# Performance work log

Hardware: AMD Instinct MI355X
Metric: run time of the kernel (lower is better)

The kernel has to match this reference:

```python
import jax, jax.numpy as jnp
import numpy as np

B, S, D_MODEL = 8, 1024, 512
DIM_K = DIM_V = 512
N_HEADS = 8
DK = DIM_K // N_HEADS
DV = DIM_V // N_HEADS
NORM = 1.0 / np.sqrt(D_MODEL).astype(np.float32)  # note: 1/sqrt(d_model), per source


def setup_inputs() -> dict:
    key = jax.random.key(0)
    ks = jax.random.split(key, 6)
    s = 0.05  # small init to keep softmax well-conditioned
    return {
        "x": jax.random.normal(ks[0], (B, S, D_MODEL), jnp.float32),
        "y": jax.random.normal(ks[1], (B, S, D_MODEL), jnp.float32),
        "q_w": jax.random.normal(ks[2], (D_MODEL, DIM_K), jnp.float32) * s,
        "q_b": jnp.zeros((DIM_K,), jnp.float32),
        "k_w": jax.random.normal(ks[3], (D_MODEL, DIM_K), jnp.float32) * s,
        "k_b": jnp.zeros((DIM_K,), jnp.float32),
        "v_w": jax.random.normal(ks[4], (D_MODEL, DIM_V), jnp.float32) * s,
        "v_b": jnp.zeros((DIM_V,), jnp.float32),
        "o_w": jax.random.normal(ks[5], (DIM_V, D_MODEL), jnp.float32) * s,
        "o_b": jnp.zeros((D_MODEL,), jnp.float32),
    }


def reference(x, y, q_w, q_b, k_w, k_b, v_w, v_b, o_w, o_b):
    b, s, _ = x.shape
    # Faithful to torch: plain row-major reshape (B,S,dim) -> (H,B,S,dh),
    # NOT a per-token head split.
    Q = (x @ q_w + q_b).reshape(N_HEADS, b, s, DK)
    K = (y @ k_w + k_b).reshape(N_HEADS, b, s, DK)
    V = (y @ v_w + v_b).reshape(N_HEADS, b, s, DV)
    scores = jnp.einsum("hbqd,hbkd->hbqk", Q, K) * NORM  # [H,B,S,S]
    # dynamic mean-threshold mask: keep only scores strictly above row mean
    thre = jnp.mean(scores, axis=-1, keepdims=True)
    scores = jnp.where(scores > thre, scores, -jnp.inf)
    attn = jax.nn.softmax(scores, axis=-1)
    out = jnp.einsum("hbqk,hbkd->hbqd", attn, V).reshape(b, s, DIM_V)
    return out @ o_w + o_b
```

## Files before the change

kernel.cpp:

```cpp
#include <hip/hip_runtime.h>
#include <hip/hip_bf16.h>
#include <hip/hip_fp16.h>


typedef _Float16 f16;
typedef __attribute__((ext_vector_type(4))) _Float16 f16x4;
typedef __attribute__((ext_vector_type(8))) _Float16 f16x8;
typedef __attribute__((ext_vector_type(8))) short bf16x8;
typedef __attribute__((ext_vector_type(4))) float f32x4;

#define MFMA16(a, b, c) __builtin_amdgcn_mfma_f32_16x16x32_f16((a), (b), (c), 0, 0, 0)
#define MFMAB16(a, b, c) __builtin_amdgcn_mfma_f32_16x16x32_bf16((a), (b), (c), 0, 0, 0)
#define MFMAPV(a, b, c) __builtin_amdgcn_mfma_f32_16x16x16f16((a), (b), (c), 0, 0, 0)

#if defined(__has_builtin) && __has_builtin(__builtin_amdgcn_exp2f)
#define EXPFN(x) __builtin_amdgcn_exp2f(x)
#define QPROJ_SCALE (0.04419417382415922f * 1.4426950408889634f)
#else
#define EXPFN(x) __expf(x)
#define QPROJ_SCALE 0.04419417382415922f
#endif

#define GLL16(gp, lp)                                       \
  __builtin_amdgcn_global_load_lds(                         \
      (const __attribute__((address_space(1))) void*)(gp),  \
      (__attribute__((address_space(3))) void*)(lp), 16, 0, 0)

__device__ __forceinline__ float b2f(short s) {
  return __uint_as_float(((unsigned)(unsigned short)s) << 16);
}

__device__ __forceinline__ void splitbf(float v, short& h, short& l) {
  unsigned short hu = __bfloat16_as_ushort(__float2bfloat16(v));
  h = (short)hu;
  float hf = __uint_as_float(((unsigned)hu) << 16);
  l = (short)__bfloat16_as_ushort(__float2bfloat16(v - hf));
}

__global__ void k_wt(const float* __restrict__ w0, const float* __restrict__ w1,
                     const float* __restrict__ w2, const float* __restrict__ w3,
                     short* __restrict__ qh, short* __restrict__ ql,
                     short* __restrict__ kh, short* __restrict__ kl,
                     f16* __restrict__ vt, f16* __restrict__ ot) {
  const float* W;
  switch (blockIdx.z) {
    case 0: W = w0; break;
    case 1: W = w1; break;
    case 2: W = w2; break;
    default: W = w3; break;
  }
  __shared__ float t[32][33];
  int bx = blockIdx.x, by = blockIdx.y;
  int tx = threadIdx.x, ty = threadIdx.y;
#pragma unroll
  for (int i = 0; i < 32; i += 8)
    t[ty + i][tx] = W[(size_t)(by * 32 + ty + i) * 512 + bx * 32 + tx];
  __syncthreads();
#pragma unroll
  for (int i = 0; i < 32; i += 8) {
    size_t idx = (size_t)(bx * 32 + ty + i) * 512 + by * 32 + tx;
    float v = t[tx][ty + i];
    if (blockIdx.z < 2) {
      short h, l;
      splitbf(v, h, l);
      if (blockIdx.z == 0) { qh[idx] = h; ql[idx] = l; }
      else { kh[idx] = h; kl[idx] = l; }
    } else {
      if (blockIdx.z == 2) vt[idx] = (f16)v;
      else ot[idx] = (f16)v;
    }
  }
}

__global__ __launch_bounds__(256) void k_split(
    const float* __restrict__ x, const float* __restrict__ y,
    short* __restrict__ Xh, short* __restrict__ Xl, short* __restrict__ Yh,
    short* __restrict__ Yl, f16* __restrict__ Ym) {
  const float* src = blockIdx.y ? y : x;
  short* dh = blockIdx.y ? Yh : Xh;
  short* dl = blockIdx.y ? Yl : Xl;
  const size_t i = ((size_t)blockIdx.x * 256 + threadIdx.x) * 8;
  float4 a = *(const float4*)(src + i);
  float4 b = *(const float4*)(src + i + 4);
  float v[8] = {a.x, a.y, a.z, a.w, b.x, b.y, b.z, b.w};
  bf16x8 h, l;
#pragma unroll
  for (int j = 0; j < 8; ++j) {
    short hh, ll;
    splitbf(v[j], hh, ll);
    h[j] = hh;
    l[j] = ll;
  }
  *(bf16x8*)(dh + i) = h;
  *(bf16x8*)(dl + i) = l;
  if (blockIdx.y) {
    f16x8 m8;
#pragma unroll
    for (int j = 0; j < 8; ++j) m8[j] = (f16)v[j];
    *(f16x8*)(Ym + i) = m8;
  }
}

#define GSTAGE(buf, kk)                                              \
  {                                                                  \
    _Pragma("unroll") for (int j = 0; j < 4; ++j) {                  \
      const int rowu = half + j * 16;                                \
      const int row = rowu + srow;                                   \
      const int slog = sslot ^ ((row >> 1) & 3);                     \
      GLL16(gsb + (size_t)(rb + row) * 512 + (kk) + slog * 8,        \
            &ldsb[buf][rowu][0]);                                    \
    }                                                                \
  }

template <typename OT>
__device__ __forceinline__ void gemm16_gll(const f16* __restrict__ A,
                                           const f16* __restrict__ WT,
                                           const float* __restrict__ bias,
                                           OT* __restrict__ C, int m0, int n0,
                                           f16 (*As)[128][32],
                                           f16 (*Bs)[128][32]) {
  const int tid = threadIdx.x;
  const int wv = tid >> 6, lane = tid & 63;
  const int wm = wv >> 1, wn = wv & 1;
  const int l15 = lane & 15, lg = lane >> 4;
  const int srow = lane >> 2, sslot = lane & 3;

  const f16* gsb = (wv < 2) ? A : WT;
  const int rb = (wv < 2) ? m0 : n0;
  f16(*ldsb)[128][32] = (wv < 2) ? As : Bs;
  const int half = (wv & 1) * 64;

  const f32x4 fz = {0.f, 0.f, 0.f, 0.f};
  f32x4 acc[4][4];
#pragma unroll
  for (int m = 0; m < 4; ++m)
#pragma unroll
    for (int n = 0; n < 4; ++n) acc[m][n] = fz;

  GSTAGE(0, 0);
  int cur = 0;
  for (int k0 = 0; k0 < 512; k0 += 32) {
    __syncthreads();
    if (k0 < 480) GSTAGE(cur ^ 1, k0 + 32);
    f16x8 af[4], bf[4];
#pragma unroll
    for (int m = 0; m < 4; ++m) {
      const int r = wm * 64 + m * 16 + l15;
      af[m] = *(const f16x8*)&As[cur][r][(lg ^ ((r >> 1) & 3)) * 8];
    }
#pragma unroll
    for (int n = 0; n < 4; ++n) {
      const int r = wn * 64 + n * 16 + l15;
      bf[n] = *(const f16x8*)&Bs[cur][r][(lg ^ ((r >> 1) & 3)) * 8];
    }
#pragma unroll
    for (int m = 0; m < 4; ++m)
#pragma unroll
      for (int n = 0; n < 4; ++n) acc[m][n] = MFMA16(af[m], bf[n], acc[m][n]);
    cur ^= 1;
  }
#pragma unroll
  for (int n = 0; n < 4; ++n) {
    const int col = n0 + wn * 64 + n * 16 + l15;
    const float b = bias[col];
#pragma unroll
    for (int m = 0; m < 4; ++m) {
      const int row = m0 + wm * 64 + m * 16 + lg * 4;
#pragma unroll
      for (int r = 0; r < 4; ++r)
        C[(size_t)(row + r) * 512 + col] = (OT)(acc[m][n][r] + b);
    }
  }
}

__global__ __launch_bounds__(256) void k_gemm_out(const f16* __restrict__ Om,
                                                  const f16* __restrict__ owT,
                                                  const float* __restrict__ ob,
                                                  float* __restrict__ out) {
  __shared__ __align__(16) f16 As[2][128][32];
  __shared__ __align__(16) f16 Bs[2][128][32];
  const int lid = blockIdx.x + (blockIdx.y << 2);
  const int swz = ((lid & 7) << 5) + (lid >> 3);
  gemm16_gll<float>(Om, owT, ob, out, (swz >> 2) * 128, (swz & 3) * 128, As,
                    Bs);
}

#define PSTAGE(buf, kk)                                             \
  {                                                                 \
    _Pragma("unroll") for (int j = 0; j < 8; ++j) {                 \
      const int row = j * 16 + srow;                                \
      const int slog = sslot ^ ((row >> 1) & 3);                    \
      GLL16(gsb + (size_t)(rb + row) * 512 + (kk) + slog * 8,       \
            &sm4[buf][wv][j * 16][0]);                              \
    }                                                               \
  }

__global__ __launch_bounds__(256) void k_proj(
    const short* __restrict__ Xh, const short* __restrict__ Xl,
    const short* __restrict__ Yh, const short* __restrict__ Yl,
    const f16* __restrict__ Ym, const short* __restrict__ qwh,
    const short* __restrict__ qwl, const short* __restrict__ kwh,
    const short* __restrict__ kwl, const f16* __restrict__ vwT,
    const float* __restrict__ qb, const float* __restrict__ kbias,
    const float* __restrict__ vb, short* __restrict__ Qh,
    short* __restrict__ Ql, short* __restrict__ Kh, short* __restrict__ Kl,
    f16* __restrict__ Vm, float* __restrict__ Kpart) {
  __shared__ __align__(16) short sm4[2][4][128][32];
  const int lid = blockIdx.x + (blockIdx.y << 2);
  const int swz = ((lid & 7) << 5) + (lid >> 3);
  const int nt = swz & 3, mt = swz >> 2;
  const int m0 = mt * 128, n0 = nt * 128;
  const int z = blockIdx.z;
  if (z == 2) {
    gemm16_gll<f16>(Ym, vwT, vb, Vm, m0, n0, (f16(*)[128][32]) & sm4[0][0][0][0],
                    (f16(*)[128][32]) & sm4[0][2][0][0]);
    return;
  }
  const short* Agh = z ? Yh : Xh;
  const short* Agl = z ? Yl : Xl;
  const short* Wh = z ? kwh : qwh;
  const short* Wl = z ? kwl : qwl;
  const float* bias = z ? kbias : qb;
  short* Ch = z ? Kh : Qh;
  short* Cl = z ? Kl : Ql;
  const float osc = z ? 1.f : (float)QPROJ_SCALE;

  const int tid = threadIdx.x;
  const int wv = tid >> 6, lane = tid & 63;
  const int wm = wv >> 1, wn = wv & 1;
  const int l15 = lane & 15, lg = lane >> 4;
  const int srow = lane >> 2, sslot = lane & 3;

  const short* gsb = (wv == 0) ? Agh : (wv == 1) ? Agl : (wv == 2) ? Wh : Wl;
  const int rb = (wv < 2) ? m0 : n0;

  const f32x4 fz = {0.f, 0.f, 0.f, 0.f};
  f32x4 acc[4][4];
#pragma unroll
  for (int m = 0; m < 4; ++m)
#pragma unroll
    for (int n = 0; n < 4; ++n) acc[m][n] = fz;

  PSTAGE(0, 0);
  int cur = 0;
  for (int k0 = 0; k0 < 512; k0 += 32) {
    __syncthreads();
    if (k0 < 480) PSTAGE(cur ^ 1, k0 + 32);
    bf16x8 afh[4], afl[4], bfh[4], bfl[4];
#pragma unroll
    for (int m = 0; m < 4; ++m) {
      const int r = wm * 64 + m * 16 + l15;
      const int sl = (lg ^ ((r >> 1) & 3)) * 8;
      afh[m] = *(const bf16x8*)&sm4[cur][0][r][sl];
      afl[m] = *(const bf16x8*)&sm4[cur][1][r][sl];
    }
#pragma unroll
    for (int n = 0; n < 4; ++n) {
      const int r = wn * 64 + n * 16 + l15;
      const int sl = (lg ^ ((r >> 1) & 3)) * 8;
      bfh[n] = *(const bf16x8*)&sm4[cur][2][r][sl];
      bfl[n] = *(const bf16x8*)&sm4[cur][3][r][sl];
    }
#pragma unroll
    for (int m = 0; m < 4; ++m)
#pragma unroll
      for (int n = 0; n < 4; ++n) {
        acc[m][n] = MFMAB16(afh[m], bfh[n], acc[m][n]);
        acc[m][n] = MFMAB16(afh[m], bfl[n], acc[m][n]);
        acc[m][n] = MFMAB16(afl[m], bfh[n], acc[m][n]);
      }
    cur ^= 1;
  }
  float csum[4];
#pragma unroll
  for (int n = 0; n < 4; ++n) {
    const int col = n0 + wn * 64 + n * 16 + l15;
    const float b = bias[col];
    csum[n] = 16.f * b;
#pragma unroll
    for (int m = 0; m < 4; ++m) {
      const int row = m0 + wm * 64 + m * 16 + lg * 4;
#pragma unroll
      for (int r = 0; r < 4; ++r) {
        const float vraw = acc[m][n][r] + b;
        csum[n] += acc[m][n][r];
        short h, l;
        splitbf(vraw * osc, h, l);
        const size_t idx = (size_t)(row + r) * 512 + col;
        Ch[idx] = h;
        Cl[idx] = l;
      }
    }
  }
  if (z == 1) {
    float* cred = (float*)&sm4[0][0][0][0];
    __syncthreads();
#pragma unroll
    for (int n = 0; n < 4; ++n)
      cred[(wn * 64 + n * 16 + l15) * 8 + wm * 4 + lg] = csum[n];
    __syncthreads();
    if (tid < 64) {
      float s = 0.f;
#pragma unroll
      for (int j = 0; j < 8; ++j)
        s += cred[tid * 8 + j] + cred[(tid + 64) * 8 + j];
      Kpart[((size_t)mt * 4 + nt) * 64 + tid] = s;
    }
  }
}

__global__ __launch_bounds__(256) void k_vtr(const f16* __restrict__ Vm,
                                             f16* __restrict__ Vt) {
  const int p = blockIdx.y;
  const int j0 = blockIdx.x * 16;
  __shared__ f16 L[16][520];
  const int tid = threadIdx.x;
#pragma unroll
  for (int it = 0; it < 4; ++it) {
    int idx = it * 256 + tid;
    int row = idx >> 6, oct = idx & 63;
    *(f16x8*)&L[row][oct * 8] =
        *(const f16x8*)&Vm[(size_t)(p * 128 + j0 + row) * 512 + oct * 8];
  }
  __syncthreads();
#pragma unroll
  for (int it = 0; it < 4; ++it) {
    int idx = it * 256 + tid;
    int dh = idx >> 4, j = idx & 15;
    f16x8 v;
#pragma unroll
    for (int g = 0; g < 8; ++g) v[g] = L[j][g * 64 + dh];
    *(f16x8*)&Vt[((size_t)p * 64 + dh) * 1024 + (j0 + j) * 8] = v;
  }
}

#define LOADREG(cc)                              \
  {                                              \
    rh = *(const bf16x8*)(KhSrc + (cc) * 4096);  \
    rl = *(const bf16x8*)(KlSrc + (cc) * 4096);  \
    rv = *(const f16x8*)(VSrc + (cc) * 64);      \
  }
#define STOREBUF(b)                      \
  {                                      \
    *(bf16x8*)&KhS[b][skey][sslot] = rh; \
    *(bf16x8*)&KlS[b][skey][sslot] = rl; \
    *(f16x8*)&Vs[b][skey][sslot] = rv;   \
  }

#define CHUNK(cb_, c_)                                                        \
  {                                                                           \
    __syncthreads();                                                          \
    if ((c_) < 15) STOREBUF((cb_) ^ 1);             \
    if ((c_) < 14) LOADREG((c_) + 2);                                         \
    __builtin_amdgcn_s_setprio(1);                                            \
    f32x4 aa[4];                                                              \
    _Pragma("unroll") for (int t = 0; t < 4; ++t) {                           \
      const int krow = t * 16 + l15;                                          \
      const int ksw = l15 & 7;                           \
      bf16x8 kh0 = *(const bf16x8*)&KhS[cb_][krow][(lg ^ ksw) * 8];           \
      bf16x8 kh1 = *(const bf16x8*)&KhS[cb_][krow][((4 + lg) ^ ksw) * 8];     \
      bf16x8 kl0 = *(const bf16x8*)&KlS[cb_][krow][(lg ^ ksw) * 8];           \
      bf16x8 kl1 = *(const bf16x8*)&KlS[cb_][krow][((4 + lg) ^ ksw) * 8];     \
      f32x4 s1 = fz, s2 = fz;                                                 \
      s1 = MFMAB16(kh0, qh0, s1);                                             \
      s2 = MFMAB16(kh1, qh1, s2);                                             \
      s1 = MFMAB16(kl0, qh0, s1);                                             \
      s2 = MFMAB16(kl1, qh1, s2);                                             \
      s1 = MFMAB16(kh0, ql0, s1);                                             \
      s2 = MFMAB16(kh1, ql1, s2);                                             \
      aa[t] = s1 + s2;                                                        \
    }                                                                         \
    f16x4 va[4][4];                                                           \
    _Pragma("unroll") for (int d0 = 0; d0 < 4; ++d0) {                        \
      const int vrow = d0 * 16 + l15;                                         \
      const int vsw = l15 & 7;                                                \
      _Pragma("unroll") for (int t = 0; t < 4; ++t)                           \
        va[d0][t] = *(const f16x4*)&Vs[cb_][vrow]                             \
                        [(((t * 2 + (lg >> 1)) ^ vsw) * 8) + (lg & 1) * 4];   \
    }                                                                         \
    f16x4 pf[4];                                                              \
    _Pragma("unroll") for (int t = 0; t < 4; ++t)                             \
      _Pragma("unroll") for (int r = 0; r < 4; ++r) {                         \
        float v = aa[t][r];                                                   \
        pf[t][r] = (f16)((v > sm) ? EXPFN(v) : 0.f);                          \
      }                                                                       \
    _Pragma("unroll") for (int t = 0; t < 4; ++t) {                           \
      od = MFMAPV(kones, pf[t], od);                                          \
      _Pragma("unroll") for (int d0 = 0; d0 < 4; ++d0)                        \
        oac[d0] = MFMAPV(va[d0][t], pf[t], oac[d0]);                          \
    }                                                                         \
    __builtin_amdgcn_s_setprio(0);                                            \
  }

__global__ __launch_bounds__(512, 4) void k_attn(
    const short* __restrict__ Qh, const short* __restrict__ Ql,
    const short* __restrict__ Kh, const short* __restrict__ Kl,
    const f16* __restrict__ Vt, const float* __restrict__ Kpart,
    f16* __restrict__ Om) {
  constexpr int S = 1024, DH = 64;
  const int p = blockIdx.x;
  const int qt = blockIdx.y;
  const size_t pb = (size_t)p * S * DH;
  const short* Qhp = Qh + pb;
  const short* Qlp = Ql + pb;
  const short* Khp = Kh + pb;
  const short* Klp = Kl + pb;
  const f16* Vtp = Vt + pb;
  f16* Op = Om + pb;

  const int tid = threadIdx.x;
  const int w = tid >> 6, lane = tid & 63;
  const int l15 = lane & 15, lg = lane >> 4;

  __shared__ __align__(16) short KhS[2][64][64];
  __shared__ __align__(16) short KlS[2][64][64];
  __shared__ __align__(16) f16 Vs[2][64][64];

  const int skey = tid >> 3;
  const int slot8 = tid & 7;
  const int sslot = (slot8 ^ (skey & 7)) * 8;
  const short* KhSrc = Khp + skey * 64 + slot8 * 8;
  const short* KlSrc = Klp + skey * 64 + slot8 * 8;
  const f16* VSrc = Vtp + (size_t)skey * 1024 + slot8 * 8;

  bf16x8 rh, rl;
  f16x8 rv;
  LOADREG(0);
  STOREBUF(0);
  LOADREG(1);

  const int qrow = qt * 128 + w * 16;
  const size_t qo = (size_t)(qrow + l15) * DH + lg * 8;
  bf16x8 qh0 = *(const bf16x8*)(Qhp + qo);
  bf16x8 ql0 = *(const bf16x8*)(Qlp + qo);
  bf16x8 qh1 = *(const bf16x8*)(Qhp + qo + 32);
  bf16x8 ql1 = *(const bf16x8*)(Qlp + qo + 32);

  const float* kp = Kpart + (size_t)p * 256;
  float km0[8], km1[8];
#pragma unroll
  for (int j = 0; j < 8; ++j) { km0[j] = 0.f; km1[j] = 0.f; }
#pragma unroll
  for (int pt = 0; pt < 4; ++pt) {
    const float* bb = kp + pt * 64;
#pragma unroll
    for (int j = 0; j < 8; ++j) {
      km0[j] += bb[lg * 8 + j];
      km1[j] += bb[32 + lg * 8 + j];
    }
  }
  float sm = 0.f;
#pragma unroll
  for (int j = 0; j < 8; ++j) {
    sm += (b2f(qh0[j]) + b2f(ql0[j])) * km0[j] +
          (b2f(qh1[j]) + b2f(ql1[j])) * km1[j];
  }
  sm += __shfl_xor(sm, 16);
  sm += __shfl_xor(sm, 32);
  sm *= (1.f / 1024.f);

  const f32x4 fz = {0.f, 0.f, 0.f, 0.f};
  const f16x4 kones = {(f16)1.f, (f16)1.f, (f16)1.f, (f16)1.f};
  f32x4 oac[4];
#pragma unroll
  for (int d = 0; d < 4; ++d) oac[d] = fz;
  f32x4 od = fz;

  for (int cc = 0; cc < 16; cc += 2) {
    CHUNK(0, cc);
    CHUNK(1, cc + 1);
  }

  const float inv = 1.f / od[0];
#pragma unroll
  for (int d0 = 0; d0 < 4; ++d0) {
    f16x4 o0;
#pragma unroll
    for (int r = 0; r < 4; ++r) o0[r] = (f16)(oac[d0][r] * inv);
    *(f16x4*)&Op[(size_t)(qrow + l15) * DH + d0 * 16 + lg * 4] = o0;
  }
}

extern "C" void kernel_launch(void* const* d_in, const int* in_sizes, int n_in,
                              void* d_out, int out_size, void* d_ws,
                              size_t ws_size, hipStream_t stream) {
  const float* x = (const float*)d_in[0];
  const float* y = (const float*)d_in[1];
  const float* qw = (const float*)d_in[2];
  const float* qb = (const float*)d_in[3];
  const float* kw = (const float*)d_in[4];
  const float* kbias = (const float*)d_in[5];
  const float* vw = (const float*)d_in[6];
  const float* vb = (const float*)d_in[7];
  const float* ow = (const float*)d_in[8];
  const float* ob = (const float*)d_in[9];
  float* out = (float*)d_out;

  char* ws = (char*)d_ws;
  const size_t WT_B = 512ull * 512 * 2;
  const size_t MAT_B = 8192ull * 512 * 2;
  short* qwhT = (short*)(ws + 0 * WT_B);
  short* qwlT = (short*)(ws + 1 * WT_B);
  short* kwhT = (short*)(ws + 2 * WT_B);
  short* kwlT = (short*)(ws + 3 * WT_B);
  f16* vwT = (f16*)(ws + 4 * WT_B);
  f16* owT = (f16*)(ws + 5 * WT_B);
  char* m = ws + 6 * WT_B;
  short* Qh = (short*)(m + 0 * MAT_B);
  short* Ql = (short*)(m + 1 * MAT_B);
  short* Kh = (short*)(m + 2 * MAT_B);
  short* Kl = (short*)(m + 3 * MAT_B);
  f16* Vm = (f16*)(m + 4 * MAT_B);
  short* Xh = (short*)(m + 5 * MAT_B);
  short* Xl = (short*)(m + 6 * MAT_B);
  short* Yh = (short*)(m + 7 * MAT_B);
  short* Yl = (short*)(m + 8 * MAT_B);
  f16* Ym = (f16*)(m + 9 * MAT_B);
  float* Kpart = (float*)(m + 10 * MAT_B);
  f16* Vtr = (f16*)Xh;
  f16* Om = (f16*)Yh;

  hipLaunchKernelGGL(k_wt, dim3(16, 16, 4), dim3(32, 8), 0, stream, qw, kw, vw,
                     ow, qwhT, qwlT, kwhT, kwlT, vwT, owT);
  hipLaunchKernelGGL(k_split, dim3(2048, 2), dim3(256), 0, stream, x, y, Xh,
                     Xl, Yh, Yl, Ym);
  hipLaunchKernelGGL(k_proj, dim3(4, 64, 3), dim3(256), 0, stream, Xh, Xl, Yh,
                     Yl, Ym, qwhT, qwlT, kwhT, kwlT, vwT, qb, kbias, vb, Qh,
                     Ql, Kh, Kl, Vm, Kpart);
  hipLaunchKernelGGL(k_vtr, dim3(8, 64), dim3(256), 0, stream, Vm, Vtr);
  hipLaunchKernelGGL(k_attn, dim3(64, 8), dim3(512), 0, stream, Qh, Ql, Kh,
                     Kl, Vtr, Kpart, Om);
  hipLaunchKernelGGL(k_gemm_out, dim3(4, 64), dim3(256), 0, stream, Om, owT,
                     ob, out);
}
```

Baseline: 118.4 us.

## Fuse weight prep into split kernel, use async LDS loads in attention, retile output GEMM

Merges the weight transpose/convert kernel into the input split kernel so a single launch handles both. The attention kernel's K/V staging switches from register load-then-store to direct global-to-LDS loads, with the swizzle moved to the source address. The output GEMM moves from 128x128 to 128x64 tiles with a dedicated staging macro, doubling the block count to improve occupancy. The aims are fewer launches, lower register pressure, and better CU fill, at the cost of uneven work in the fused prep kernel.

```diff
diff --git a/kernel.cpp b/kernel.cpp
--- a/kernel.cpp
+++ b/kernel.cpp
@@ -37,49 +37,48 @@
   l = (short)__bfloat16_as_ushort(__float2bfloat16(v - hf));
 }
 
-__global__ void k_wt(const float* __restrict__ w0, const float* __restrict__ w1,
-                     const float* __restrict__ w2, const float* __restrict__ w3,
-                     short* __restrict__ qh, short* __restrict__ ql,
-                     short* __restrict__ kh, short* __restrict__ kl,
-                     f16* __restrict__ vt, f16* __restrict__ ot) {
-  const float* W;
-  switch (blockIdx.z) {
-    case 0: W = w0; break;
-    case 1: W = w1; break;
-    case 2: W = w2; break;
-    default: W = w3; break;
-  }
-  __shared__ float t[32][33];
-  int bx = blockIdx.x, by = blockIdx.y;
-  int tx = threadIdx.x, ty = threadIdx.y;
-#pragma unroll
-  for (int i = 0; i < 32; i += 8)
-    t[ty + i][tx] = W[(size_t)(by * 32 + ty + i) * 512 + bx * 32 + tx];
-  __syncthreads();
-#pragma unroll
-  for (int i = 0; i < 32; i += 8) {
-    size_t idx = (size_t)(bx * 32 + ty + i) * 512 + by * 32 + tx;
-    float v = t[tx][ty + i];
-    if (blockIdx.z < 2) {
-      short h, l;
-      splitbf(v, h, l);
-      if (blockIdx.z == 0) { qh[idx] = h; ql[idx] = l; }
-      else { kh[idx] = h; kl[idx] = l; }
-    } else {
-      if (blockIdx.z == 2) vt[idx] = (f16)v;
-      else ot[idx] = (f16)v;
-    }
-  }
-}
-
-__global__ __launch_bounds__(256) void k_split(
+__global__ __launch_bounds__(256) void k_pre(
     const float* __restrict__ x, const float* __restrict__ y,
+    const float* __restrict__ qw, const float* __restrict__ kw,
+    const float* __restrict__ vw, const float* __restrict__ ow,
+    short* __restrict__ qh, short* __restrict__ ql, short* __restrict__ kh,
+    short* __restrict__ kl, f16* __restrict__ vt, f16* __restrict__ ot,
     short* __restrict__ Xh, short* __restrict__ Xl, short* __restrict__ Yh,
     short* __restrict__ Yl, f16* __restrict__ Ym) {
-  const float* src = blockIdx.y ? y : x;
-  short* dh = blockIdx.y ? Yh : Xh;
-  short* dl = blockIdx.y ? Yl : Xl;
-  const size_t i = ((size_t)blockIdx.x * 256 + threadIdx.x) * 8;
+  const int tid = threadIdx.x;
+  const int bx = blockIdx.x;
+  const int by = blockIdx.y;
+  if (bx < 512) {
+    const int wt = by * 512 + bx;
+    const int z = wt >> 8;
+    const int tile = wt & 255;
+    const int bxx = tile & 15, byy = tile >> 4;
+    const float* W = (z == 0) ? qw : (z == 1) ? kw : (z == 2) ? vw : ow;
+    __shared__ float t[32][33];
+    const int tx = tid & 31, ty = tid >> 5;
+#pragma unroll
+    for (int i = 0; i < 32; i += 8)
+      t[ty + i][tx] = W[(size_t)(byy * 32 + ty + i) * 512 + bxx * 32 + tx];
+    __syncthreads();
+#pragma unroll
+    for (int i = 0; i < 32; i += 8) {
+      size_t idx = (size_t)(bxx * 32 + ty + i) * 512 + byy * 32 + tx;
+      float v = t[tx][ty + i];
+      if (z < 2) {
+        short h, l;
+        splitbf(v, h, l);
+        if (z == 0) { qh[idx] = h; ql[idx] = l; }
+        else { kh[idx] = h; kl[idx] = l; }
+      } else {
+        if (z == 2) vt[idx] = (f16)v;
+        else ot[idx] = (f16)v;
+      }
+    }
+  }
+  const float* src = by ? y : x;
+  short* dh = by ? Yh : Xh;
+  short* dl = by ? Yl : Xl;
+  const size_t i = ((size_t)bx * 256 + tid) * 8;
   float4 a = *(const float4*)(src + i);
   float4 b = *(const float4*)(src + i + 4);
   float v[8] = {a.x, a.y, a.z, a.w, b.x, b.y, b.z, b.w};
@@ -93,7 +92,7 @@
   }
   *(bf16x8*)(dh + i) = h;
   *(bf16x8*)(dl + i) = l;
-  if (blockIdx.y) {
+  if (by) {
     f16x8 m8;
 #pragma unroll
     for (int j = 0; j < 8; ++j) m8[j] = (f16)v[j];
@@ -173,16 +172,83 @@
   }
 }
 
+#define OSTAGE(buf, kk)                                                       \
+  {                                                                           \
+    if (wv < 2) {                                                             \
+      _Pragma("unroll") for (int j = 0; j < 4; ++j) {                         \
+        const int rowu = wv * 64 + j * 16;                                    \
+        const int row = rowu + srow;                                          \
+        const int slog = sslot ^ ((row >> 1) & 3);                            \
+        GLL16(Om + (size_t)(m0 + row) * 512 + (kk) + slog * 8,                \
+              &As[buf][rowu][0]);                                             \
+      }                                                                       \
+    } else {                                                                  \
+      _Pragma("unroll") for (int j = 0; j < 2; ++j) {                         \
+        const int rowu = (wv - 2) * 32 + j * 16;                              \
+        const int row = rowu + srow;                                          \
+        const int slog = sslot ^ ((row >> 1) & 3);                            \
+        GLL16(owT + (size_t)(n0 + row) * 512 + (kk) + slog * 8,               \
+              &Bs[buf][rowu][0]);                                             \
+      }                                                                       \
+    }                                                                         \
+  }
+
 __global__ __launch_bounds__(256) void k_gemm_out(const f16* __restrict__ Om,
                                                   const f16* __restrict__ owT,
                                                   const float* __restrict__ ob,
                                                   float* __restrict__ out) {
   __shared__ __align__(16) f16 As[2][128][32];
-  __shared__ __align__(16) f16 Bs[2][128][32];
-  const int lid = blockIdx.x + (blockIdx.y << 2);
-  const int swz = ((lid & 7) << 5) + (lid >> 3);
-  gemm16_gll<float>(Om, owT, ob, out, (swz >> 2) * 128, (swz & 3) * 128, As,
-                    Bs);
+  __shared__ __align__(16) f16 Bs[2][64][32];
+  const int lid = blockIdx.x + (blockIdx.y << 3);
+  const int swz = ((lid & 7) << 6) + (lid >> 3);
+  const int m0 = (swz >> 3) * 128, n0 = (swz & 7) * 64;
+  const int tid = threadIdx.x;
+  const int wv = tid >> 6, lane = tid & 63;
+  const int wm = wv >> 1, wn = wv & 1;
+  const int l15 = lane & 15, lg = lane >> 4;
+  const int srow = lane >> 2, sslot = lane & 3;
+
+  const f32x4 fz = {0.f, 0.f, 0.f, 0.f};
+  f32x4 acc[4][2];
+#pragma unroll
+  for (int m = 0; m < 4; ++m)
+#pragma unroll
+    for (int n = 0; n < 2; ++n) acc[m][n] = fz;
+
+  OSTAGE(0, 0);
+  int cur = 0;
+  for (int k0 = 0; k0 < 512; k0 += 32) {
+    __syncthreads();
+    if (k0 < 480) OSTAGE(cur ^ 1, k0 + 32);
+    f16x8 af[4], bf[2];
+#pragma unroll
+    for (int m = 0; m < 4; ++m) {
+      const int r = wm * 64 + m * 16 + l15;
+      af[m] = *(const f16x8*)&As[cur][r][(lg ^ ((r >> 1) & 3)) * 8];
+    }
+#pragma unroll
+    for (int n = 0; n < 2; ++n) {
+      const int r = wn * 32 + n * 16 + l15;
+      bf[n] = *(const f16x8*)&Bs[cur][r][(lg ^ ((r >> 1) & 3)) * 8];
+    }
+#pragma unroll
+    for (int m = 0; m < 4; ++m)
+#pragma unroll
+      for (int n = 0; n < 2; ++n) acc[m][n] = MFMA16(af[m], bf[n], acc[m][n]);
+    cur ^= 1;
+  }
+#pragma unroll
+  for (int n = 0; n < 2; ++n) {
+    const int col = n0 + wn * 32 + n * 16 + l15;
+    const float b = ob[col];
+#pragma unroll
+    for (int m = 0; m < 4; ++m) {
+      const int row = m0 + wm * 64 + m * 16 + lg * 4;
+#pragma unroll
+      for (int r = 0; r < 4; ++r)
+        out[(size_t)(row + r) * 512 + col] = acc[m][n][r] + b;
+    }
+  }
 }
 
 #define PSTAGE(buf, kk)                                             \
@@ -334,24 +400,17 @@
   }
 }
 
-#define LOADREG(cc)                              \
-  {                                              \
-    rh = *(const bf16x8*)(KhSrc + (cc) * 4096);  \
-    rl = *(const bf16x8*)(KlSrc + (cc) * 4096);  \
-    rv = *(const f16x8*)(VSrc + (cc) * 64);      \
-  }
-#define STOREBUF(b)                      \
-  {                                      \
-    *(bf16x8*)&KhS[b][skey][sslot] = rh; \
-    *(bf16x8*)&KlS[b][skey][sslot] = rl; \
-    *(f16x8*)&Vs[b][skey][sslot] = rv;   \
+#define STAGE(b, cc)                                       \
+  {                                                        \
+    GLL16(KhSrc + (cc) * 4096, &KhS[b][skey][slot8 * 8]);  \
+    GLL16(KlSrc + (cc) * 4096, &KlS[b][skey][slot8 * 8]);  \
+    GLL16(VSrc + (cc) * 64, &Vs[b][skey][slot8 * 8]);      \
   }
 
 #define CHUNK(cb_, c_)                                                        \
   {                                                                           \
-    __syncthreads();                                                          \
-    if ((c_) < 15) STOREBUF((cb_) ^ 1);             \
-    if ((c_) < 14) LOADREG((c_) + 2);                                         \
+    __syncthreads();       \
+    if ((c_) < 15) STAGE((cb_) ^ 1, (c_) + 1);       \
     __builtin_amdgcn_s_setprio(1);                                            \
     f32x4 aa[4];                                                              \
     _Pragma("unroll") for (int t = 0; t < 4; ++t) {                           \
@@ -418,16 +477,12 @@
 
   const int skey = tid >> 3;
   const int slot8 = tid & 7;
-  const int sslot = (slot8 ^ (skey & 7)) * 8;
-  const short* KhSrc = Khp + skey * 64 + slot8 * 8;
-  const short* KlSrc = Klp + skey * 64 + slot8 * 8;
-  const f16* VSrc = Vtp + (size_t)skey * 1024 + slot8 * 8;
-
-  bf16x8 rh, rl;
-  f16x8 rv;
-  LOADREG(0);
-  STOREBUF(0);
-  LOADREG(1);
+  const int ssw = skey & 7;
+  const short* KhSrc = Khp + skey * 64 + (slot8 ^ ssw) * 8;
+  const short* KlSrc = Klp + skey * 64 + (slot8 ^ ssw) * 8;
+  const f16* VSrc = Vtp + (size_t)skey * 1024 + (slot8 ^ ssw) * 8;
+
+  STAGE(0, 0);
 
   const int qrow = qt * 128 + w * 16;
   const size_t qo = (size_t)(qrow + l15) * DH + lg * 8;
@@ -520,16 +575,15 @@
   f16* Vtr = (f16*)Xh;
   f16* Om = (f16*)Yh;
 
-  hipLaunchKernelGGL(k_wt, dim3(16, 16, 4), dim3(32, 8), 0, stream, qw, kw, vw,
-                     ow, qwhT, qwlT, kwhT, kwlT, vwT, owT);
-  hipLaunchKernelGGL(k_split, dim3(2048, 2), dim3(256), 0, stream, x, y, Xh,
-                     Xl, Yh, Yl, Ym);
+  hipLaunchKernelGGL(k_pre, dim3(2048, 2), dim3(256), 0, stream, x, y, qw, kw,
+                     vw, ow, qwhT, qwlT, kwhT, kwlT, vwT, owT, Xh, Xl, Yh, Yl,
+                     Ym);
   hipLaunchKernelGGL(k_proj, dim3(4, 64, 3), dim3(256), 0, stream, Xh, Xl, Yh,
                      Yl, Ym, qwhT, qwlT, kwhT, kwlT, vwT, qb, kbias, vb, Qh,
                      Ql, Kh, Kl, Vm, Kpart);
   hipLaunchKernelGGL(k_vtr, dim3(8, 64), dim3(256), 0, stream, Vm, Vtr);
   hipLaunchKernelGGL(k_attn, dim3(64, 8), dim3(512), 0, stream, Qh, Ql, Kh,
                      Kl, Vtr, Kpart, Om);
-  hipLaunchKernelGGL(k_gemm_out, dim3(4, 64), dim3(256), 0, stream, Om, owT,
+  hipLaunchKernelGGL(k_gemm_out, dim3(8, 64), dim3(256), 0, stream, Om, owT,
                      ob, out);
 }
```

New measurement: 116.1 us. 1.02x faster.
